# Kernel optimization log

Measured on AMD Instinct MI355X. Metric: run time of the kernel, lower is better.

The kernel has to match this reference:

```python
import jax, jax.numpy as jnp
import numpy as np

EPS = 1e-8
THRESHOLD = 0.5  # ternary quantization threshold

IN_FEATURES = 4096
OUT_FEATURES = 4096


def setup_inputs() -> dict:
    key = jax.random.key(0)
    k_x, k_w, k_b = jax.random.split(key, 3)
    x = jax.random.normal(k_x, (2, 2048, IN_FEATURES), dtype=jnp.float32)
    # xavier_uniform init for weight (out, in)
    limit = float(np.sqrt(6.0 / (IN_FEATURES + OUT_FEATURES)))
    weight = jax.random.uniform(k_w, (OUT_FEATURES, IN_FEATURES), dtype=jnp.float32,
                                minval=-limit, maxval=limit)
    bias = jnp.zeros((OUT_FEATURES,), dtype=jnp.float32)
    return {"x": x, "weight": weight, "bias": bias}


def ternary_quantize(w):
    # scale = mean(|w|), clamped; quantize to {-1,0,1} with 0.5 threshold
    scale = jnp.maximum(jnp.mean(jnp.abs(w)), EPS)
    w_norm = w / scale
    q = jnp.sign(w_norm) * (jnp.abs(w_norm) > THRESHOLD).astype(w.dtype)
    return q, scale


def reference(x, weight, bias):
    # eval-mode forward of BitNetLinear (ternary mode, activation scaling on)
    qw, scale = ternary_quantize(weight)
    input_scale = jnp.maximum(jnp.mean(jnp.abs(x)), EPS)
    scaled_x = x / input_scale
    # F.linear: y = x @ W^T + b, with dequantized weight qw*scale
    out = jnp.einsum('bsi,oi->bso', scaled_x, qw * scale) + bias
    return out * input_scale
```

## Files before the change

kernel.cpp:

```cpp
#include <hip/hip_runtime.h>
#include <hip/hip_bf16.h>

#define AS1 __attribute__((address_space(1)))
#define AS3 __attribute__((address_space(3)))

typedef __attribute__((ext_vector_type(8))) short bfrag8;
typedef __attribute__((ext_vector_type(4))) float floatx4;

static constexpr int M = 4096, N = 4096, K = 4096;
static constexpr long long NELEM = 16777216LL;
static constexpr int PB = 1024;

__device__ __forceinline__ unsigned short f2bf(float f) {
    unsigned int u = __float_as_uint(f);
    u += 0x7FFFu + ((u >> 16) & 1u);
    return (unsigned short)(u >> 16);
}

__device__ __forceinline__ unsigned short tq(float v, float scale_f) {
    float wn = v / scale_f;
    if (fabsf(wn) > 0.5f)
        return (unsigned short)(0x3F80u | ((__float_as_uint(v) >> 16) & 0x8000u));
    return 0;
}

__device__ __forceinline__ double block_reduce(double s) {
    #pragma unroll
    for (int off = 32; off > 0; off >>= 1) s += __shfl_down(s, off, 64);
    __shared__ double part[4];
    int lane = threadIdx.x & 63, wv = threadIdx.x >> 6;
    if (lane == 0) part[wv] = s;
    __syncthreads();
    return part[0] + part[1] + part[2] + part[3];
}

__device__ __forceinline__ void block_reduce2_bcast(double& a, double& b) {
    #pragma unroll
    for (int off = 32; off > 0; off >>= 1) {
        a += __shfl_down(a, off, 64);
        b += __shfl_down(b, off, 64);
    }
    __shared__ double pa[4], pb[4];
    int lane = threadIdx.x & 63, wv = threadIdx.x >> 6;
    if (lane == 0) { pa[wv] = a; pb[wv] = b; }
    __syncthreads();
    a = pa[0] + pa[1] + pa[2] + pa[3];
    b = pb[0] + pb[1] + pb[2] + pb[3];
}

__global__ __launch_bounds__(256) void prep_reduce(
        const float* __restrict__ x, unsigned short* __restrict__ xb,
        const float* __restrict__ w,
        double* __restrict__ px, double* __restrict__ pw) {
    const int b = blockIdx.x;
    const bool isW = b >= PB;
    const int rb = isW ? b - PB : b;
    const float4* src = (const float4*)(isW ? w : x);
    const long long base = (long long)rb * 4096 + threadIdx.x;

    float4 v[16];
    #pragma unroll
    for (int i = 0; i < 16; i++) v[i] = src[base + i * 256];

    double s = 0.0;
    #pragma unroll
    for (int i = 0; i < 16; i++) {
        s += (double)fabsf(v[i].x); s += (double)fabsf(v[i].y);
        s += (double)fabsf(v[i].z); s += (double)fabsf(v[i].w);
    }

    if (!isW) {
        ushort4* xb4 = (ushort4*)xb;
        #pragma unroll
        for (int i = 0; i < 16; i++) {
            ushort4 r;
            r.x = f2bf(v[i].x); r.y = f2bf(v[i].y);
            r.z = f2bf(v[i].z); r.w = f2bf(v[i].w);
            xb4[base + i * 256] = r;
        }
    }

    double bs = block_reduce(s);
    if (threadIdx.x == 0) (isW ? pw : px)[rb] = bs;
}

__global__ __launch_bounds__(256) void quantize_w(
        const float* __restrict__ w, unsigned short* __restrict__ qb,
        const double* __restrict__ px, const double* __restrict__ pw,
        float* __restrict__ scales) {
    const int t = threadIdx.x;
    double sx = 0.0, sw = 0.0;
    #pragma unroll
    for (int i = 0; i < 4; i++) { sx += px[t + i * 256]; sw += pw[t + i * 256]; }
    block_reduce2_bcast(sx, sw);
    const float scale_w = (float)fmax(sw / (double)NELEM, 1e-8);
    const float scale_x = (float)fmax(sx / (double)NELEM, 1e-8);
    if (blockIdx.x == 0 && t == 0) { scales[0] = scale_w; scales[1] = scale_x; }

    const float4* w4 = (const float4*)w;
    ushort4* q4 = (ushort4*)qb;
    const long long base = (long long)blockIdx.x * 4096 + t;
    float4 v[16];
    #pragma unroll
    for (int i = 0; i < 16; i++) v[i] = w4[base + i * 256];
    #pragma unroll
    for (int i = 0; i < 16; i++) {
        ushort4 r;
        r.x = tq(v[i].x, scale_w); r.y = tq(v[i].y, scale_w);
        r.z = tq(v[i].z, scale_w); r.w = tq(v[i].w, scale_w);
        q4[base + i * 256] = r;
    }
}

__global__ __launch_bounds__(512, 2) void gemm_bt256(
        const unsigned short* __restrict__ A,
        const unsigned short* __restrict__ B,
        const float* __restrict__ bias,
        const float* __restrict__ scales,
        float* __restrict__ out) {
    __shared__ alignas(16) char lds[131072];

    const int tid = threadIdx.x;
    const int lane = tid & 63;
    const int wv = tid >> 6;
    const int wm = wv & 1;
    const int wn = wv >> 1;
    const int col16 = lane & 15;
    const int quad  = lane >> 4;

    const int bid = blockIdx.x;
    const int swz = (bid & 7) * 32 + (bid >> 3);
    const int bx = swz & 15;
    const int by = swz >> 4;
    const int m0 = by * 256;
    const int n0 = bx * 256;

    const int srow8  = lane >> 3;
    const int schunk = (lane & 7) ^ srow8;
    const int scol   = schunk * 8;

    floatx4 acc[8][4];
    #pragma unroll
    for (int i = 0; i < 8; i++)
        #pragma unroll
        for (int j = 0; j < 4; j++)
            acc[i][j] = (floatx4)0.0f;

    char* ldsc = (char*)lds;

    auto stage4 = [&](const unsigned short* __restrict__ gmat, int base0,
                      char* region, long long k0) {
        #pragma unroll
        for (int h = 0; h < 2; ++h)
            #pragma unroll
            for (int l = 0; l < 2; ++l) {
                const int c = wv * 2 + l;
                const unsigned short* g = gmat
                    + (size_t)(base0 + h * 128 + c * 8 + srow8) * (size_t)K
                    + (size_t)k0 + scol;
                char* d = region + h * 16384 + c * 1024 + lane * 16;
                __builtin_amdgcn_global_load_lds((const AS1 void*)g, (AS3 void*)d, 16, 0, 0);
            }
    };

    stage4(A, m0, ldsc,                 0);
    stage4(B, n0, ldsc + 32768,         0);
    stage4(A, m0, ldsc + 65536,         64);
    stage4(B, n0, ldsc + 65536 + 32768, 64);
    asm volatile("s_waitcnt vmcnt(8)" ::: "memory");
    __builtin_amdgcn_s_barrier();

    auto tile_body = [&](const char* bufc, char* bufn, int t) {
        const bool doStage = (t >= 1) && (t < 63);
        const long long knext = (long long)(t + 1) * 64;
        const char* bA = bufc;
        const char* bB = bufc + 32768;

        bfrag8 bf[4][2];
        #pragma unroll
        for (int j = 0; j < 4; ++j) {
            const int rB = wn * 64 + j * 16 + col16;
            #pragma unroll
            for (int kk = 0; kk < 2; ++kk)
                bf[j][kk] = *(const bfrag8*)(bB + rB * 128 +
                                (((kk * 4 + quad) ^ (col16 & 7)) << 4));
        }

        #pragma unroll
        for (int q = 0; q < 4; ++q) {
            bfrag8 af[2][2];
            #pragma unroll
            for (int di = 0; di < 2; ++di) {
                const int rA = wm * 128 + (q * 2 + di) * 16 + col16;
                #pragma unroll
                for (int kk = 0; kk < 2; ++kk)
                    af[di][kk] = *(const bfrag8*)(bA + rA * 128 +
                                    (((kk * 4 + quad) ^ (col16 & 7)) << 4));
            }
            if (q == 0 && doStage) stage4(B, n0, bufn + 32768, knext);
            if (q == 1 && doStage) stage4(A, m0, bufn, knext);

            __builtin_amdgcn_s_barrier();
            asm volatile("s_waitcnt lgkmcnt(0)" ::: "memory");
            __builtin_amdgcn_s_setprio(1);
            #pragma unroll
            for (int di = 0; di < 2; ++di)
                #pragma unroll
                for (int j = 0; j < 4; ++j) {
                    acc[q * 2 + di][j] = __builtin_amdgcn_mfma_f32_16x16x32_bf16(
                        af[di][0], bf[j][0], acc[q * 2 + di][j], 0, 0, 0);
                    acc[q * 2 + di][j] = __builtin_amdgcn_mfma_f32_16x16x32_bf16(
                        af[di][1], bf[j][1], acc[q * 2 + di][j], 0, 0, 0);
                }
            __builtin_amdgcn_s_setprio(0);
            if (q == 3) asm volatile("s_waitcnt vmcnt(0)" ::: "memory");
            __builtin_amdgcn_s_barrier();
        }
    };

    for (int t2 = 0; t2 < 32; ++t2) {
        tile_body(ldsc,         ldsc + 65536, 2 * t2);
        tile_body(ldsc + 65536, ldsc,         2 * t2 + 1);
    }

    const float wscale = scales[0];
    const float iscale = scales[1];

    float bv[4];
    #pragma unroll
    for (int j = 0; j < 4; ++j)
        bv[j] = bias[n0 + wn * 64 + j * 16 + col16] * iscale;

    #pragma unroll
    for (int i = 0; i < 8; ++i) {
        const int mbase = m0 + wm * 128 + i * 16 + quad * 4;
        #pragma unroll
        for (int j = 0; j < 4; ++j) {
            const int n = n0 + wn * 64 + j * 16 + col16;
            #pragma unroll
            for (int r = 0; r < 4; ++r)
                out[(size_t)(mbase + r) * N + n] = acc[i][j][r] * wscale + bv[j];
        }
    }
}

extern "C" void kernel_launch(void* const* d_in, const int* in_sizes, int n_in,
                              void* d_out, int out_size, void* d_ws, size_t ws_size,
                              hipStream_t stream) {
    const float* x    = (const float*)d_in[0];
    const float* w    = (const float*)d_in[1];
    const float* bias = (const float*)d_in[2];
    float* out = (float*)d_out;

    char* ws = (char*)d_ws;
    float*  scales = (float*)ws;
    double* px     = (double*)(ws + 256);
    double* pw     = (double*)(ws + 256 + PB * 8);
    unsigned short* xb = (unsigned short*)(ws + 16640);
    unsigned short* qb = (unsigned short*)(ws + 16640 + (size_t)NELEM * 2);

    prep_reduce<<<2 * PB, 256, 0, stream>>>(x, xb, w, px, pw);
    quantize_w<<<PB, 256, 0, stream>>>(w, qb, px, pw, scales);

    gemm_bt256<<<dim3(256), 512, 0, stream>>>(xb, qb, bias, scales, out);
}
```

Before: 339.3 us.

## Stage B tile two steps ahead and split loads into halves across quarters

Restructures the GEMM main-loop prefetch schedule. A for the next tile is loaded in two halves during quarters 0-1, and B for the tile after next is loaded into the current buffer's B region during quarters 2-3, since B fragments are already in registers. The end-of-tile wait becomes vmcnt(4) instead of vmcnt(0), so the latest B loads can stay in flight across the tile boundary. This deepens the pipeline and spreads global loads more evenly, at the cost of tighter reasoning about buffer reuse and wait counts.

```diff
diff --git a/kernel.cpp b/kernel.cpp
--- a/kernel.cpp
+++ b/kernel.cpp
@@ -146,33 +146,36 @@
         for (int j = 0; j < 4; j++)
             acc[i][j] = (floatx4)0.0f;
 
-    char* ldsc = (char*)lds;
-
-    auto stage4 = [&](const unsigned short* __restrict__ gmat, int base0,
-                      char* region, long long k0) {
-        #pragma unroll
-        for (int h = 0; h < 2; ++h)
-            #pragma unroll
-            for (int l = 0; l < 2; ++l) {
-                const int c = wv * 2 + l;
-                const unsigned short* g = gmat
-                    + (size_t)(base0 + h * 128 + c * 8 + srow8) * (size_t)K
-                    + (size_t)k0 + scol;
-                char* d = region + h * 16384 + c * 1024 + lane * 16;
-                __builtin_amdgcn_global_load_lds((const AS1 void*)g, (AS3 void*)d, 16, 0, 0);
-            }
+    char* buf0 = (char*)lds;
+    char* buf1 = (char*)lds + 65536;
+
+    auto stage_half = [&](const unsigned short* __restrict__ gmat, int base0,
+                          char* region, long long k0, int h) {
+        #pragma unroll
+        for (int l = 0; l < 2; ++l) {
+            const int c = wv * 2 + l;
+            const unsigned short* g = gmat
+                + (size_t)(base0 + h * 128 + c * 8 + srow8) * (size_t)K
+                + (size_t)k0 + scol;
+            char* d = region + h * 16384 + c * 1024 + lane * 16;
+            __builtin_amdgcn_global_load_lds((const AS1 void*)g, (AS3 void*)d, 16, 0, 0);
+        }
     };
 
-    stage4(A, m0, ldsc,                 0);
-    stage4(B, n0, ldsc + 32768,         0);
-    stage4(A, m0, ldsc + 65536,         64);
-    stage4(B, n0, ldsc + 65536 + 32768, 64);
-    asm volatile("s_waitcnt vmcnt(8)" ::: "memory");
+    stage_half(B, n0, buf0 + 32768, 0, 0);
+    stage_half(B, n0, buf0 + 32768, 0, 1);
+    stage_half(A, m0, buf0,         0, 0);
+    stage_half(A, m0, buf0,         0, 1);
+    stage_half(B, n0, buf1 + 32768, 64, 0);
+    stage_half(B, n0, buf1 + 32768, 64, 1);
+    asm volatile("s_waitcnt vmcnt(4)" ::: "memory");
     __builtin_amdgcn_s_barrier();
 
-    auto tile_body = [&](const char* bufc, char* bufn, int t) {
-        const bool doStage = (t >= 1) && (t < 63);
-        const long long knext = (long long)(t + 1) * 64;
+    auto tile_body = [&](char* bufc, char* bufn, int t) {
+        const bool stA = (t + 1) < 64;
+        const bool stB = (t + 2) < 64;
+        const long long kA = (long long)(t + 1) * 64;
+        const long long kB = (long long)(t + 2) * 64;
         const char* bA = bufc;
         const char* bB = bufc + 32768;
 
@@ -197,8 +200,10 @@
                     af[di][kk] = *(const bfrag8*)(bA + rA * 128 +
                                     (((kk * 4 + quad) ^ (col16 & 7)) << 4));
             }
-            if (q == 0 && doStage) stage4(B, n0, bufn + 32768, knext);
-            if (q == 1 && doStage) stage4(A, m0, bufn, knext);
+            if (q == 0 && stA) stage_half(A, m0, bufn, kA, 0);
+            if (q == 1 && stA) stage_half(A, m0, bufn, kA, 1);
+            if (q == 2 && stB) stage_half(B, n0, bufc + 32768, kB, 0);
+            if (q == 3 && stB) stage_half(B, n0, bufc + 32768, kB, 1);
 
             __builtin_amdgcn_s_barrier();
             asm volatile("s_waitcnt lgkmcnt(0)" ::: "memory");
@@ -213,14 +218,14 @@
                         af[di][1], bf[j][1], acc[q * 2 + di][j], 0, 0, 0);
                 }
             __builtin_amdgcn_s_setprio(0);
-            if (q == 3) asm volatile("s_waitcnt vmcnt(0)" ::: "memory");
+            if (q == 3) asm volatile("s_waitcnt vmcnt(4)" ::: "memory");
             __builtin_amdgcn_s_barrier();
         }
     };
 
     for (int t2 = 0; t2 < 32; ++t2) {
-        tile_body(ldsc,         ldsc + 65536, 2 * t2);
-        tile_body(ldsc + 65536, ldsc,         2 * t2 + 1);
+        tile_body(buf0, buf1, 2 * t2);
+        tile_body(buf1, buf0, 2 * t2 + 1);
     }
 
     const float wscale = scales[0];
```

After: 287.5 us. -15.3%, faster.

## Deepen GEMM prefetch to triple-buffered A with two-tile-ahead loads

Applied to the files above, without the earlier changes.

The GEMM main loop now triple-buffers the A tile and double-buffers B in LDS (160 KB), issuing global-to-LDS loads two k-tiles ahead instead of one. Loads are split into four half-tile stages spread across the four MFMA sub-steps, and the per-tile wait relaxes from vmcnt(0) to vmcnt(8) so a tile's loads can remain in flight across barriers. The aim is to hide more global memory latency. The larger LDS footprint may drop occupancy from two blocks per CU to one, and reusing B buffers while their loads are still in flight needs correct wait ordering.

```diff
diff --git a/kernel.cpp b/kernel.cpp
--- a/kernel.cpp
+++ b/kernel.cpp
@@ -118,7 +118,7 @@
         const float* __restrict__ bias,
         const float* __restrict__ scales,
         float* __restrict__ out) {
-    __shared__ alignas(16) char lds[131072];
+    __shared__ alignas(16) char lds[163840];
 
     const int tid = threadIdx.x;
     const int lane = tid & 63;
@@ -146,35 +146,38 @@
         for (int j = 0; j < 4; j++)
             acc[i][j] = (floatx4)0.0f;
 
-    char* ldsc = (char*)lds;
-
-    auto stage4 = [&](const unsigned short* __restrict__ gmat, int base0,
-                      char* region, long long k0) {
-        #pragma unroll
-        for (int h = 0; h < 2; ++h)
-            #pragma unroll
-            for (int l = 0; l < 2; ++l) {
-                const int c = wv * 2 + l;
-                const unsigned short* g = gmat
-                    + (size_t)(base0 + h * 128 + c * 8 + srow8) * (size_t)K
-                    + (size_t)k0 + scol;
-                char* d = region + h * 16384 + c * 1024 + lane * 16;
-                __builtin_amdgcn_global_load_lds((const AS1 void*)g, (AS3 void*)d, 16, 0, 0);
-            }
+    char* const A0 = (char*)lds;
+    char* const A1 = (char*)lds + 32768;
+    char* const A2 = (char*)lds + 65536;
+    char* const B0 = (char*)lds + 98304;
+    char* const B1 = (char*)lds + 131072;
+
+    auto stage_half = [&](const unsigned short* __restrict__ gmat, int base0,
+                          char* region, long long k0, int h) {
+        #pragma unroll
+        for (int l = 0; l < 2; ++l) {
+            const int c = wv * 2 + l;
+            const unsigned short* g = gmat
+                + (size_t)(base0 + h * 128 + c * 8 + srow8) * (size_t)K
+                + (size_t)k0 + scol;
+            char* d = region + h * 16384 + c * 1024 + lane * 16;
+            __builtin_amdgcn_global_load_lds((const AS1 void*)g, (AS3 void*)d, 16, 0, 0);
+        }
     };
 
-    stage4(A, m0, ldsc,                 0);
-    stage4(B, n0, ldsc + 32768,         0);
-    stage4(A, m0, ldsc + 65536,         64);
-    stage4(B, n0, ldsc + 65536 + 32768, 64);
+    stage_half(A, m0, A0, 0,  0);
+    stage_half(A, m0, A0, 0,  1);
+    stage_half(B, n0, B0, 0,  0);
+    stage_half(B, n0, B0, 0,  1);
+    stage_half(A, m0, A1, 64, 0);
+    stage_half(A, m0, A1, 64, 1);
+    stage_half(B, n0, B1, 64, 0);
+    stage_half(B, n0, B1, 64, 1);
     asm volatile("s_waitcnt vmcnt(8)" ::: "memory");
     __builtin_amdgcn_s_barrier();
 
-    auto tile_body = [&](const char* bufc, char* bufn, int t) {
-        const bool doStage = (t >= 1) && (t < 63);
-        const long long knext = (long long)(t + 1) * 64;
-        const char* bA = bufc;
-        const char* bB = bufc + 32768;
+    auto tile_body = [&](char* bA, char* bB, char* aT, int t, bool st, int wait_mode) {
+        const long long kN = (long long)(t + 2) * 64;
 
         bfrag8 bf[4][2];
         #pragma unroll
@@ -197,8 +200,10 @@
                     af[di][kk] = *(const bfrag8*)(bA + rA * 128 +
                                     (((kk * 4 + quad) ^ (col16 & 7)) << 4));
             }
-            if (q == 0 && doStage) stage4(B, n0, bufn + 32768, knext);
-            if (q == 1 && doStage) stage4(A, m0, bufn, knext);
+            if (q == 0 && st) stage_half(A, m0, aT, kN, 0);
+            if (q == 1 && st) stage_half(A, m0, aT, kN, 1);
+            if (q == 2 && st) stage_half(B, n0, bB, kN, 0);
+            if (q == 3 && st) stage_half(B, n0, bB, kN, 1);
 
             __builtin_amdgcn_s_barrier();
             asm volatile("s_waitcnt lgkmcnt(0)" ::: "memory");
@@ -213,15 +218,27 @@
                         af[di][1], bf[j][1], acc[q * 2 + di][j], 0, 0, 0);
                 }
             __builtin_amdgcn_s_setprio(0);
-            if (q == 3) asm volatile("s_waitcnt vmcnt(0)" ::: "memory");
+            if (q == 3) {
+                if (wait_mode == 0)      asm volatile("s_waitcnt vmcnt(8)" ::: "memory");
+                else if (wait_mode == 1) asm volatile("s_waitcnt vmcnt(0)" ::: "memory");
+            }
             __builtin_amdgcn_s_barrier();
         }
     };
 
-    for (int t2 = 0; t2 < 32; ++t2) {
-        tile_body(ldsc,         ldsc + 65536, 2 * t2);
-        tile_body(ldsc + 65536, ldsc,         2 * t2 + 1);
-    }
+    for (int t6 = 0; t6 < 10; ++t6) {
+        const int tb = t6 * 6;
+        tile_body(A0, B0, A2, tb + 0, true, 0);
+        tile_body(A1, B1, A0, tb + 1, true, 0);
+        tile_body(A2, B0, A1, tb + 2, true, 0);
+        tile_body(A0, B1, A2, tb + 3, true, 0);
+        tile_body(A1, B0, A0, tb + 4, true, 0);
+        tile_body(A2, B1, A1, tb + 5, true, 0);
+    }
+    tile_body(A0, B0, A2, 60, true,  0);
+    tile_body(A1, B1, A0, 61, true,  0);
+    tile_body(A2, B0, A1, 62, false, 1);
+    tile_body(A0, B1, A2, 63, false, 2);
 
     const float wscale = scales[0];
     const float iscale = scales[1];
```

Result: faster. 302.0 us (-11.0%).
